# Performance work log

Measured on AMD Instinct MI355X. Metric: run time of the kernel, lower is better.

## Reference

```python
import jax, jax.numpy as jnp
from jax import lax
import numpy as np

B, H, W, C = 8, 56, 56, 384
NUM_HEADS, HEAD_CH = 6, 64
BN_EPS = 1e-5
DN = ('NHWC', 'HWIO', 'NHWC')


def conv_proj(x, dw_kernel, bn_scale, bn_bias, bn_mean, bn_var, pw_kernel, stride):
    """Depthwise conv -> BatchNorm (eval) -> 1x1 pointwise conv, all SAME padding."""
    in_ch = x.shape[-1]
    x = lax.conv_general_dilated(x, dw_kernel, (stride, stride), 'SAME',
                                 dimension_numbers=DN, feature_group_count=in_ch)
    x = (x - bn_mean) * (bn_scale / jnp.sqrt(bn_var + BN_EPS)) + bn_bias
    x = lax.conv_general_dilated(x, pw_kernel, (1, 1), 'SAME', dimension_numbers=DN)
    return x


def setup_inputs() -> dict:
    key = jax.random.key(0)
    ks = jax.random.split(key, 16)
    d = {
        'inputs_q': jax.random.normal(ks[0], (B, H, W, C), jnp.float32),
        'inputs_kv': jax.random.normal(ks[1], (B, H, W, C), jnp.float32),
        'out_kernel': jax.random.normal(ks[2], (NUM_HEADS, HEAD_CH, C), jnp.float32) * 0.05,
    }
    for i, p in enumerate(['q', 'k', 'v']):
        d[f'{p}_dw_kernel'] = jax.random.normal(ks[3 + i], (3, 3, 1, C), jnp.float32) * 0.1
        d[f'{p}_bn_scale'] = jnp.ones((C,), jnp.float32)
        d[f'{p}_bn_bias'] = jnp.zeros((C,), jnp.float32)
        d[f'{p}_bn_mean'] = jnp.zeros((C,), jnp.float32)
        d[f'{p}_bn_var'] = jnp.ones((C,), jnp.float32)
        d[f'{p}_pw_kernel'] = jax.random.normal(ks[6 + i], (1, 1, C, NUM_HEADS * HEAD_CH), jnp.float32) * 0.05
    return d


def reference(inputs_q, inputs_kv,
              q_dw_kernel, q_bn_scale, q_bn_bias, q_bn_mean, q_bn_var, q_pw_kernel,
              k_dw_kernel, k_bn_scale, k_bn_bias, k_bn_mean, k_bn_var, k_pw_kernel,
              v_dw_kernel, v_bn_scale, v_bn_bias, v_bn_mean, v_bn_var, v_pw_kernel,
              out_kernel):
    q = conv_proj(inputs_q, q_dw_kernel, q_bn_scale, q_bn_bias, q_bn_mean, q_bn_var, q_pw_kernel, 1)
    k = conv_proj(inputs_kv, k_dw_kernel, k_bn_scale, k_bn_bias, k_bn_mean, k_bn_var, k_pw_kernel, 2)
    v = conv_proj(inputs_kv, v_dw_kernel, v_bn_scale, v_bn_bias, v_bn_mean, v_bn_var, v_pw_kernel, 2)

    def to_tokens(x):  # [b,H,W,h*d] -> [b,HW,h,d]
        b, hh, ww, _ = x.shape
        return x.reshape(b, hh * ww, NUM_HEADS, HEAD_CH)

    q = to_tokens(q) / jnp.sqrt(jnp.float32(HEAD_CH))
    k = to_tokens(k)
    v = to_tokens(v)

    attn = jnp.einsum('bqhd,bkhd->bhqk', q, k)       # [b,h,Nq,Nkv]
    attn = jax.nn.softmax(attn, axis=-1)
    out = jnp.einsum('bhqk,bkhd->bqhd', attn, v)     # [b,Nq,h,d]
    out = jnp.einsum('bqhd,hdo->bqo', out, out_kernel)  # DenseGeneral over (h,d)
    return out
```

## Files before the change

kernel.cpp:

```cpp
#include <hip/hip_runtime.h>
#include <hip/hip_bf16.h>
#include <hip/hip_fp16.h>

#define BB 8
#define HH 56
#define WW 56
#define CC 384
#define NHD 6
#define DD 64
#define HK 28
#define WK 28
#define NQ (HH*WW)
#define NKV (HK*WK)
#define NTOK (BB*NQ)
#define NTOKKV (BB*NKV)
#define BN_EPS 1e-5f
#define LOG2E 1.44269504f

typedef _Float16 f16;
typedef _Float16 f16x2 __attribute__((ext_vector_type(2)));
typedef _Float16 f16x4 __attribute__((ext_vector_type(4)));
typedef _Float16 f16x8 __attribute__((ext_vector_type(8)));
typedef float f32x4 __attribute__((ext_vector_type(4)));

__device__ __forceinline__ float fast_exp2(float x) {
#if __has_builtin(__builtin_amdgcn_exp2f)
  return __builtin_amdgcn_exp2f(x);
#else
  return __expf(x * 0.69314718056f);
#endif
}

__device__ __forceinline__ f16x4 pack4(float p0, float p1, float p2, float p3) {
#if __has_builtin(__builtin_amdgcn_cvt_pkrtz)
  f16x2 a = __builtin_bit_cast(f16x2, __builtin_amdgcn_cvt_pkrtz(p0, p1));
  f16x2 b = __builtin_bit_cast(f16x2, __builtin_amdgcn_cvt_pkrtz(p2, p3));
  return __builtin_shufflevector(a, b, 0, 1, 2, 3);
#else
  f16x4 r; r[0] = (f16)p0; r[1] = (f16)p1; r[2] = (f16)p2; r[3] = (f16)p3;
  return r;
#endif
}

__device__ __forceinline__ void dw_s1_body(
    int blk, int tid, const float* __restrict__ in, const float* __restrict__ w,
    const float* __restrict__ bns, const float* __restrict__ bnb,
    const float* __restrict__ bnm, const float* __restrict__ bnv,
    f16* __restrict__ out) {
  int idx = blk * 256 + tid;
  int pp = idx / 96;
  int c = (idx % 96) * 4;
  int b = pp / (HH * WK);
  int rem = pp % (HH * WK);
  int y = rem / WK, xh = rem % WK;
  int x0 = xh * 2;
  float a0x = 0, a0y = 0, a0z = 0, a0w = 0;
  float a1x = 0, a1y = 0, a1z = 0, a1w = 0;
#pragma unroll
  for (int kh = 0; kh < 3; ++kh) {
    int iy = y + kh - 1;
    if ((unsigned)iy >= (unsigned)HH) continue;
    const float* rp = in + ((size_t)(b * HH + iy) * WW) * CC + c;
    const float4 z4 = {0.f, 0.f, 0.f, 0.f};
    const float4 v0 = (x0 > 0) ? *(const float4*)(rp + (size_t)(x0 - 1) * CC) : z4;
    const float4 v1 = *(const float4*)(rp + (size_t)x0 * CC);
    const float4 v2 = *(const float4*)(rp + (size_t)(x0 + 1) * CC);
    const float4 v3 = (x0 < 54) ? *(const float4*)(rp + (size_t)(x0 + 2) * CC) : z4;
    const float4 w0 = *(const float4*)(w + (kh * 3 + 0) * CC + c);
    const float4 w1 = *(const float4*)(w + (kh * 3 + 1) * CC + c);
    const float4 w2 = *(const float4*)(w + (kh * 3 + 2) * CC + c);
    a0x = fmaf(v0.x, w0.x, fmaf(v1.x, w1.x, fmaf(v2.x, w2.x, a0x)));
    a0y = fmaf(v0.y, w0.y, fmaf(v1.y, w1.y, fmaf(v2.y, w2.y, a0y)));
    a0z = fmaf(v0.z, w0.z, fmaf(v1.z, w1.z, fmaf(v2.z, w2.z, a0z)));
    a0w = fmaf(v0.w, w0.w, fmaf(v1.w, w1.w, fmaf(v2.w, w2.w, a0w)));
    a1x = fmaf(v1.x, w0.x, fmaf(v2.x, w1.x, fmaf(v3.x, w2.x, a1x)));
    a1y = fmaf(v1.y, w0.y, fmaf(v2.y, w1.y, fmaf(v3.y, w2.y, a1y)));
    a1z = fmaf(v1.z, w0.z, fmaf(v2.z, w1.z, fmaf(v3.z, w2.z, a1z)));
    a1w = fmaf(v1.w, w0.w, fmaf(v2.w, w1.w, fmaf(v3.w, w2.w, a1w)));
  }
  const float4 s = *(const float4*)(bns + c);
  const float4 bi = *(const float4*)(bnb + c);
  const float4 m = *(const float4*)(bnm + c);
  const float4 va = *(const float4*)(bnv + c);
  f16x4 r0, r1;
  float g;
  g = s.x * rsqrtf(va.x + BN_EPS); r0[0] = (f16)fmaf(a0x - m.x, g, bi.x); r1[0] = (f16)fmaf(a1x - m.x, g, bi.x);
  g = s.y * rsqrtf(va.y + BN_EPS); r0[1] = (f16)fmaf(a0y - m.y, g, bi.y); r1[1] = (f16)fmaf(a1y - m.y, g, bi.y);
  g = s.z * rsqrtf(va.z + BN_EPS); r0[2] = (f16)fmaf(a0z - m.z, g, bi.z); r1[2] = (f16)fmaf(a1z - m.z, g, bi.z);
  g = s.w * rsqrtf(va.w + BN_EPS); r0[3] = (f16)fmaf(a0w - m.w, g, bi.w); r1[3] = (f16)fmaf(a1w - m.w, g, bi.w);
  const size_t pix0 = (size_t)b * NQ + y * WW + x0;
  *(f16x4*)(out + pix0 * CC + c) = r0;
  *(f16x4*)(out + (pix0 + 1) * CC + c) = r1;
}

__device__ __forceinline__ void dw_s2_body(
    int blk, int tid, const float* __restrict__ in,
    const float* __restrict__ wk_, const float* __restrict__ kbs, const float* __restrict__ kbb,
    const float* __restrict__ kbm, const float* __restrict__ kbv,
    const float* __restrict__ wv_, const float* __restrict__ vbs, const float* __restrict__ vbb,
    const float* __restrict__ vbm, const float* __restrict__ vbv,
    f16* __restrict__ outk, f16* __restrict__ outv) {
  int idx = blk * 256 + tid;
  int pix = idx / 96;
  int c = (idx % 96) * 4;
  int b = pix / (HK * WK);
  int p = pix % (HK * WK);
  int oy = p / WK, ox = p % WK;
  float kx = 0, ky = 0, kz = 0, kw4 = 0;
  float vx = 0, vy = 0, vz = 0, vw4 = 0;
#pragma unroll
  for (int kh = 0; kh < 3; ++kh) {
    int iy = oy * 2 + kh;
    if (iy >= HH) continue;
#pragma unroll
    for (int kwi = 0; kwi < 3; ++kwi) {
      int ix = ox * 2 + kwi;
      if (ix >= WW) continue;
      const float4 v = *(const float4*)(in + (((size_t)(b * HH + iy) * WW + ix) * CC + c));
      const float4 a = *(const float4*)(wk_ + ((kh * 3 + kwi) * CC + c));
      const float4 bq = *(const float4*)(wv_ + ((kh * 3 + kwi) * CC + c));
      kx = fmaf(v.x, a.x, kx); ky = fmaf(v.y, a.y, ky);
      kz = fmaf(v.z, a.z, kz); kw4 = fmaf(v.w, a.w, kw4);
      vx = fmaf(v.x, bq.x, vx); vy = fmaf(v.y, bq.y, vy);
      vz = fmaf(v.z, bq.z, vz); vw4 = fmaf(v.w, bq.w, vw4);
    }
  }
  {
    const float4 s = *(const float4*)(kbs + c);
    const float4 bi = *(const float4*)(kbb + c);
    const float4 m = *(const float4*)(kbm + c);
    const float4 va = *(const float4*)(kbv + c);
    f16x4 r; float g;
    g = s.x * rsqrtf(va.x + BN_EPS); r[0] = (f16)fmaf(kx - m.x, g, bi.x);
    g = s.y * rsqrtf(va.y + BN_EPS); r[1] = (f16)fmaf(ky - m.y, g, bi.y);
    g = s.z * rsqrtf(va.z + BN_EPS); r[2] = (f16)fmaf(kz - m.z, g, bi.z);
    g = s.w * rsqrtf(va.w + BN_EPS); r[3] = (f16)fmaf(kw4 - m.w, g, bi.w);
    *(f16x4*)(outk + (size_t)pix * CC + c) = r;
  }
  {
    const float4 s = *(const float4*)(vbs + c);
    const float4 bi = *(const float4*)(vbb + c);
    const float4 m = *(const float4*)(vbm + c);
    const float4 va = *(const float4*)(vbv + c);
    f16x4 r; float g;
    g = s.x * rsqrtf(va.x + BN_EPS); r[0] = (f16)fmaf(vx - m.x, g, bi.x);
    g = s.y * rsqrtf(va.y + BN_EPS); r[1] = (f16)fmaf(vy - m.y, g, bi.y);
    g = s.z * rsqrtf(va.z + BN_EPS); r[2] = (f16)fmaf(vz - m.z, g, bi.z);
    g = s.w * rsqrtf(va.w + BN_EPS); r[3] = (f16)fmaf(vw4 - m.w, g, bi.w);
    *(f16x4*)(outv + (size_t)pix * CC + c) = r;
  }
}

__global__ __launch_bounds__(256) void preprocess(
    const float* __restrict__ inputs_q, const float* __restrict__ inputs_kv,
    const float* __restrict__ q_dwk, const float* __restrict__ q_bs,
    const float* __restrict__ q_bb, const float* __restrict__ q_bm,
    const float* __restrict__ q_bv,
    const float* __restrict__ k_dwk, const float* __restrict__ k_bs,
    const float* __restrict__ k_bb, const float* __restrict__ k_bm,
    const float* __restrict__ k_bv,
    const float* __restrict__ v_dwk, const float* __restrict__ v_bs,
    const float* __restrict__ v_bb, const float* __restrict__ v_bm,
    const float* __restrict__ v_bv,
    const float* __restrict__ w0, const float* __restrict__ w1,
    const float* __restrict__ w2, const float* __restrict__ w3,
    f16* __restrict__ o0, f16* __restrict__ o1,
    f16* __restrict__ o2, f16* __restrict__ o3,
    f16* __restrict__ qdw, f16* __restrict__ kdw, f16* __restrict__ vdw) {
  __shared__ float t[32][33];
  const int blk = blockIdx.x;
  const int tid = threadIdx.x;
  if (blk < 4704) {
    dw_s1_body(blk, tid, inputs_q, q_dwk, q_bs, q_bb, q_bm, q_bv, qdw);
  } else if (blk < 7056) {
    dw_s2_body(blk - 4704, tid, inputs_kv,
               k_dwk, k_bs, k_bb, k_bm, k_bv,
               v_dwk, v_bs, v_bb, v_bm, v_bv, kdw, vdw);
  } else {
    const int r = blk - 7056;
    const int z = r / 144, rem = r % 144;
    const int bx = rem % 12, by = rem / 12;
    const float* src = z == 0 ? w0 : z == 1 ? w1 : z == 2 ? w2 : w3;
    f16* dst = z == 0 ? o0 : z == 1 ? o1 : z == 2 ? o2 : o3;
    const int k0 = bx * 32, n0 = by * 32;
    const int x = tid & 31, y = tid >> 5;
#pragma unroll
    for (int i = 0; i < 4; ++i) t[y + i * 8][x] = src[(size_t)(k0 + y + i * 8) * 384 + n0 + x];
    __syncthreads();
#pragma unroll
    for (int i = 0; i < 4; ++i)
      dst[(size_t)(n0 + y + i * 8) * 384 + k0 + x] = (f16)t[x][y + i * 8];
  }
}

template <int MODE>
__device__ __forceinline__ void gemm_body(
    const f16* __restrict__ A, const f16* __restrict__ Bt,
    float* __restrict__ Cf, f16* __restrict__ Ch, float scale,
    int row0, int col0) {
  __shared__ f16 As[128 * 64];
  __shared__ f16 Bs[128 * 64];
  const int tid = threadIdx.x;
  const int wave = tid >> 6, lane = tid & 63;
  const int c = lane & 15, g = lane >> 4;
  const int wr = wave >> 1, wc = wave & 1;

  const int s_base = wave * 64 + lane;
  f32x4 acc[4][4] = {};

  for (int k0 = 0; k0 < 384; k0 += 64) {
    __syncthreads();
#pragma unroll
    for (int j = 0; j < 4; ++j) {
      const int s = j * 256 + s_base;
      const int row = s >> 3, sch = s & 7;
      const int lch = sch ^ (row & 7);
      const f16* sa = A + (size_t)(row0 + row) * 384 + k0 + lch * 8;
      __builtin_amdgcn_global_load_lds(
          (const __attribute__((address_space(1))) void*)sa,
          (__attribute__((address_space(3))) void*)(As + j * 2048 + wave * 512), 16, 0, 0);
      const f16* sb = Bt + (size_t)(col0 + row) * 384 + k0 + lch * 8;
      __builtin_amdgcn_global_load_lds(
          (const __attribute__((address_space(1))) void*)sb,
          (__attribute__((address_space(3))) void*)(Bs + j * 2048 + wave * 512), 16, 0, 0);
    }
    __syncthreads();

#pragma unroll
    for (int kh = 0; kh < 2; ++kh) {
      f16x8 bf[4];
#pragma unroll
      for (int n = 0; n < 4; ++n) {
        const int row = wc * 64 + n * 16 + c;
        bf[n] = *(const f16x8*)(Bs + (size_t)row * 64 + ((kh * 4 + g) ^ (row & 7)) * 8);
      }
#pragma unroll
      for (int m = 0; m < 4; ++m) {
        const int row = wr * 64 + m * 16 + c;
        f16x8 af = *(const f16x8*)(As + (size_t)row * 64 + ((kh * 4 + g) ^ (row & 7)) * 8);
#pragma unroll
        for (int n = 0; n < 4; ++n)
          acc[m][n] = __builtin_amdgcn_mfma_f32_16x16x32_f16(af, bf[n], acc[m][n], 0, 0, 0);
      }
    }
  }

  if (MODE == 2) {
#pragma unroll
    for (int m = 0; m < 4; ++m)
#pragma unroll
      for (int n = 0; n < 4; ++n) {
        const int gr = row0 + wr * 64 + m * 16 + g * 4;
        const int col = col0 + wc * 64 + n * 16 + c;
        const int bb = gr / NKV;
        const int kv = gr - bb * NKV;
        f16x4 pk;
#pragma unroll
        for (int r = 0; r < 4; ++r) pk[r] = (f16)(acc[m][n][r] * scale);
        *(f16x4*)(Ch + ((size_t)bb * 384 + col) * NKV + kv) = pk;
      }
  } else {
#pragma unroll
    for (int m = 0; m < 4; ++m)
#pragma unroll
      for (int n = 0; n < 4; ++n)
#pragma unroll
        for (int r = 0; r < 4; ++r) {
          const size_t row = row0 + wr * 64 + m * 16 + g * 4 + r;
          const size_t col = col0 + wc * 64 + n * 16 + c;
          if (MODE == 1) Ch[row * 384 + col] = (f16)(acc[m][n][r] * scale);
          else           Cf[row * 384 + col] = acc[m][n][r] * scale;
        }
  }
}

__global__ __launch_bounds__(256) void gemm_qkv(
    const f16* __restrict__ qdw, const f16* __restrict__ wqt, f16* __restrict__ qf, float qscale,
    const f16* __restrict__ kdw, const f16* __restrict__ wkt, f16* __restrict__ kf,
    const f16* __restrict__ vdw, const f16* __restrict__ wvt, f16* __restrict__ vtp) {
  const int blk = blockIdx.x;
  if (blk < 588) {
    gemm_body<1>(qdw, wqt, nullptr, qf, qscale, (blk % 196) * 128, (blk / 196) * 128);
  } else if (blk < 735) {
    const int r = blk - 588;
    gemm_body<1>(kdw, wkt, nullptr, kf, 1.0f, (r % 49) * 128, (r / 49) * 128);
  } else {
    const int r = blk - 735;
    gemm_body<2>(vdw, wvt, nullptr, vtp, 1.0f, (r % 49) * 128, (r / 49) * 128);
  }
}

template <int MODE>
__global__ __launch_bounds__(256) void gemm_mfma(
    const f16* __restrict__ A, const f16* __restrict__ Bt,
    float* __restrict__ Cf, f16* __restrict__ Ch, float scale) {
  gemm_body<MODE>(A, Bt, Cf, Ch, scale, blockIdx.x * 128, blockIdx.y * 128);
}

__global__ __launch_bounds__(256) void attn_mfma(
    const f16* __restrict__ qp, const f16* __restrict__ kp,
    const f16* __restrict__ vt, f16* __restrict__ op) {
  __shared__ f16 Ks[64 * 64];
  __shared__ f16 Vs[64 * 64];
  __shared__ f16 Ps[4][16 * 64];
  const int bid0 = blockIdx.x;
  const int lb = (bid0 & 7) * 294 + (bid0 >> 3);
  const int qt = lb % 49;
  const int bh = lb / 49;
  const int h = bh % NHD, b = bh / NHD;
  const int tid = threadIdx.x;
  const int wave = tid >> 6, lane = tid & 63;
  const int c = lane & 15, g = lane >> 4;

  const size_t qrow = (size_t)b * NQ + qt * 64 + wave * 16 + c;
  f16x8 qa[2];
  qa[0] = *(const f16x8*)(qp + qrow * 384 + h * 64 + g * 8);
  qa[1] = *(const f16x8*)(qp + qrow * 384 + h * 64 + 32 + g * 8);

  f16x8 vones;
#pragma unroll
  for (int j = 0; j < 8; ++j) vones[j] = (f16)1.0f;

  const int tid8 = tid >> 3, tch = tid & 7;
  const int lch = tch ^ (tid8 & 7);

  const f16* kbase = kp + ((size_t)b * NKV) * 384 + h * 64;
  const f16* vbase = vt + ((size_t)(b * 384 + h * 64)) * NKV;

  float mrun = -1e30f;
  f32x4 o[4] = {};
  f32x4 osum = {};
  f16* prow = &Ps[wave][0];

  for (int ti = 0; ti < 12; ++ti) {
    const int t0 = ti * 64;
    __syncthreads();
    {
      __builtin_amdgcn_global_load_lds(
          (const __attribute__((address_space(1))) void*)(kbase + (size_t)(t0 + tid8) * 384 + lch * 8),
          (__attribute__((address_space(3))) void*)(Ks + wave * 512), 16, 0, 0);
      __builtin_amdgcn_global_load_lds(
          (const __attribute__((address_space(1))) void*)(kbase + (size_t)(t0 + 32 + tid8) * 384 + lch * 8),
          (__attribute__((address_space(3))) void*)(Ks + 2048 + wave * 512), 16, 0, 0);
      const int col = t0 + lch * 8;
      __builtin_amdgcn_global_load_lds(
          (const __attribute__((address_space(1))) void*)(vbase + (size_t)tid8 * NKV + col),
          (__attribute__((address_space(3))) void*)(Vs + wave * 512), 16, 0, 0);
      __builtin_amdgcn_global_load_lds(
          (const __attribute__((address_space(1))) void*)(vbase + (size_t)(32 + tid8) * NKV + col),
          (__attribute__((address_space(3))) void*)(Vs + 2048 + wave * 512), 16, 0, 0);
    }
    __syncthreads();

    f32x4 s[4] = {};
    __builtin_amdgcn_s_setprio(1);
#pragma unroll
    for (int kh = 0; kh < 2; ++kh) {
#pragma unroll
      for (int ct = 0; ct < 4; ++ct) {
        const int row = ct * 16 + c;
        const int sch = (kh * 4 + g) ^ (row & 7);
        f16x8 kb = *(const f16x8*)(Ks + row * 64 + sch * 8);
        s[ct] = __builtin_amdgcn_mfma_f32_16x16x32_f16(kb, qa[kh], s[ct], 0, 0, 0);
      }
    }
    __builtin_amdgcn_s_setprio(0);

    float mt = s[0][0];
#pragma unroll
    for (int ct = 0; ct < 4; ++ct)
#pragma unroll
      for (int r = 0; r < 4; ++r) mt = fmaxf(mt, s[ct][r]);
    mt = fmaxf(mt, __shfl_xor(mt, 16));
    mt = fmaxf(mt, __shfl_xor(mt, 32));

    if (__ballot(mt > mrun + 8.0f)) {
      const float mnew = fmaxf(mrun, mt);
      const float corr = fast_exp2(mrun - mnew);
      mrun = mnew;
#pragma unroll
      for (int r = 0; r < 4; ++r) {
        const float co = __shfl(corr, g * 4 + r);
#pragma unroll
        for (int dt = 0; dt < 4; ++dt) o[dt][r] *= co;
        osum[r] *= co;
      }
    }

#pragma unroll
    for (int ct = 0; ct < 4; ++ct) {
      const float p0 = fast_exp2(s[ct][0] - mrun);
      const float p1 = fast_exp2(s[ct][1] - mrun);
      const float p2 = fast_exp2(s[ct][2] - mrun);
      const float p3 = fast_exp2(s[ct][3] - mrun);
      const int sch = (ct * 2 + (g >> 1)) ^ (c & 7);
      *(f16x4*)(prow + c * 64 + sch * 8 + (g & 1) * 4) = pack4(p0, p1, p2, p3);
    }

    __builtin_amdgcn_s_setprio(1);
#pragma unroll
    for (int ks = 0; ks < 2; ++ks) {
      const int sp = (ks * 4 + g) ^ (c & 7);
      f16x8 pa = *(const f16x8*)(prow + c * 64 + sp * 8);
#pragma unroll
      for (int dt = 0; dt < 4; ++dt) {
        const int d = dt * 16 + c;
        f16x8 vb = *(const f16x8*)(Vs + d * 64 + sp * 8);
        o[dt] = __builtin_amdgcn_mfma_f32_16x16x32_f16(pa, vb, o[dt], 0, 0, 0);
      }
      osum = __builtin_amdgcn_mfma_f32_16x16x32_f16(pa, vones, osum, 0, 0, 0);
    }
    __builtin_amdgcn_s_setprio(0);
  }

  {
    const int t0 = 768;
    __syncthreads();
    {
      int kv0 = t0 + tid8; if (kv0 > NKV - 1) kv0 = NKV - 1;
      __builtin_amdgcn_global_load_lds(
          (const __attribute__((address_space(1))) void*)(kbase + (size_t)kv0 * 384 + lch * 8),
          (__attribute__((address_space(3))) void*)(Ks + wave * 512), 16, 0, 0);
      int col = t0 + lch * 8; if (col > NKV - 8) col = NKV - 8;
      __builtin_amdgcn_global_load_lds(
          (const __attribute__((address_space(1))) void*)(vbase + (size_t)tid8 * NKV + col),
          (__attribute__((address_space(3))) void*)(Vs + wave * 512), 16, 0, 0);
      __builtin_amdgcn_global_load_lds(
          (const __attribute__((address_space(1))) void*)(vbase + (size_t)(32 + tid8) * NKV + col),
          (__attribute__((address_space(3))) void*)(Vs + 2048 + wave * 512), 16, 0, 0);
    }
    __syncthreads();

    f32x4 s0 = {};
    __builtin_amdgcn_s_setprio(1);
#pragma unroll
    for (int kh = 0; kh < 2; ++kh) {
      const int sch = (kh * 4 + g) ^ (c & 7);
      f16x8 kb = *(const f16x8*)(Ks + c * 64 + sch * 8);
      s0 = __builtin_amdgcn_mfma_f32_16x16x32_f16(kb, qa[kh], s0, 0, 0, 0);
    }
    __builtin_amdgcn_s_setprio(0);

    float mt = fmaxf(fmaxf(s0[0], s0[1]), fmaxf(s0[2], s0[3]));
    mt = fmaxf(mt, __shfl_xor(mt, 16));
    mt = fmaxf(mt, __shfl_xor(mt, 32));
    if (__ballot(mt > mrun + 8.0f)) {
      const float mnew = fmaxf(mrun, mt);
      const float corr = fast_exp2(mrun - mnew);
      mrun = mnew;
#pragma unroll
      for (int r = 0; r < 4; ++r) {
        const float co = __shfl(corr, g * 4 + r);
#pragma unroll
        for (int dt = 0; dt < 4; ++dt) o[dt][r] *= co;
        osum[r] *= co;
      }
    }

    {
      const float p0 = fast_exp2(s0[0] - mrun);
      const float p1 = fast_exp2(s0[1] - mrun);
      const float p2 = fast_exp2(s0[2] - mrun);
      const float p3 = fast_exp2(s0[3] - mrun);
      const int sch0 = (0 + (g >> 1)) ^ (c & 7);
      *(f16x4*)(prow + c * 64 + sch0 * 8 + (g & 1) * 4) = pack4(p0, p1, p2, p3);
      const int sch1 = (2 + (g >> 1)) ^ (c & 7);
      f16x4 z = {};
      *(f16x4*)(prow + c * 64 + sch1 * 8 + (g & 1) * 4) = z;
    }

    __builtin_amdgcn_s_setprio(1);
    {
      const int sp = g ^ (c & 7);
      f16x8 pa = *(const f16x8*)(prow + c * 64 + sp * 8);
#pragma unroll
      for (int dt = 0; dt < 4; ++dt) {
        const int d = dt * 16 + c;
        f16x8 vb = *(const f16x8*)(Vs + d * 64 + sp * 8);
        o[dt] = __builtin_amdgcn_mfma_f32_16x16x32_f16(pa, vb, o[dt], 0, 0, 0);
      }
      osum = __builtin_amdgcn_mfma_f32_16x16x32_f16(pa, vones, osum, 0, 0, 0);
    }
    __builtin_amdgcn_s_setprio(0);
  }

  f16* obase = op + ((size_t)(b * NQ + qt * 64 + wave * 16)) * 384 + h * 64;
#pragma unroll
  for (int r = 0; r < 4; ++r) {
    const float iv = 1.0f / osum[r];
#pragma unroll
    for (int dt = 0; dt < 4; ++dt)
      obase[(size_t)(g * 4 + r) * 384 + dt * 16 + c] = (f16)(o[dt][r] * iv);
  }
}

extern "C" void kernel_launch(void* const* d_in, const int* in_sizes, int n_in,
                              void* d_out, int out_size, void* d_ws, size_t ws_size,
                              hipStream_t stream) {
  const float* inputs_q  = (const float*)d_in[0];
  const float* inputs_kv = (const float*)d_in[1];
  const float* out_kern  = (const float*)d_in[2];
  const float* q_dwk = (const float*)d_in[3];
  const float* q_bs  = (const float*)d_in[4];
  const float* q_bb  = (const float*)d_in[5];
  const float* q_bm  = (const float*)d_in[6];
  const float* q_bv  = (const float*)d_in[7];
  const float* q_pwk = (const float*)d_in[8];
  const float* k_dwk = (const float*)d_in[9];
  const float* k_bs  = (const float*)d_in[10];
  const float* k_bb  = (const float*)d_in[11];
  const float* k_bm  = (const float*)d_in[12];
  const float* k_bv  = (const float*)d_in[13];
  const float* k_pwk = (const float*)d_in[14];
  const float* v_dwk = (const float*)d_in[15];
  const float* v_bs  = (const float*)d_in[16];
  const float* v_bb  = (const float*)d_in[17];
  const float* v_bm  = (const float*)d_in[18];
  const float* v_bv  = (const float*)d_in[19];
  const float* v_pwk = (const float*)d_in[20];

  char* wsb = (char*)d_ws;
  f16* qdw = (f16*)(wsb + 0);
  f16* kdw = (f16*)(wsb + 19267584);
  f16* vdw = (f16*)(wsb + 24084480);
  f16* qf  = (f16*)(wsb + 28901376);
  f16* kf  = (f16*)(wsb + 48168960);
  f16* vtp = (f16*)(wsb + 57802752);
  f16* of  = (f16*)(wsb + 62619648);
  f16* wqt = (f16*)(wsb + 81887232);
  f16* wkt = (f16*)(wsb + 82182144);
  f16* wvt = (f16*)(wsb + 82477056);
  f16* wot = (f16*)(wsb + 82771968);

  preprocess<<<7632, 256, 0, stream>>>(
      inputs_q, inputs_kv,
      q_dwk, q_bs, q_bb, q_bm, q_bv,
      k_dwk, k_bs, k_bb, k_bm, k_bv,
      v_dwk, v_bs, v_bb, v_bm, v_bv,
      q_pwk, k_pwk, v_pwk, out_kern, wqt, wkt, wvt, wot,
      qdw, kdw, vdw);
  gemm_qkv<<<882, 256, 0, stream>>>(qdw, wqt, qf, 0.125f * LOG2E,
                                    kdw, wkt, kf, vdw, wvt, vtp);
  attn_mfma<<<BB * NHD * 49, 256, 0, stream>>>(qf, kf, vtp, of);
  gemm_mfma<0><<<dim3(196, 3), 256, 0, stream>>>(of, wot, (float*)d_out, nullptr, 1.0f);
}
```

Measured before the change: 150.2 us.

## Register-prefetch next K/V tile during attention compute instead of direct LDS loads

Replaces the synchronous global_load_lds staging of each K/V tile with a register-staged software pipeline. The next tile's K and V are loaded into registers while the current tile is computed, then written to LDS at the start of the next iteration. The tail tile is folded into the loop as iteration 13 with clamped indices. The aim is to hide global-load latency behind the MFMA and softmax work, at the cost of extra VGPRs and explicit LDS stores.

```diff
diff --git a/kernel.cpp b/kernel.cpp
--- a/kernel.cpp
+++ b/kernel.cpp
@@ -332,156 +332,143 @@
   f32x4 osum = {};
   f16* prow = &Ps[wave][0];
 
-  for (int ti = 0; ti < 12; ++ti) {
-    const int t0 = ti * 64;
+  f16x8 kr0, kr1, vr0, vr1;
+  kr0 = *(const f16x8*)(kbase + (size_t)tid8 * 384 + lch * 8);
+  kr1 = *(const f16x8*)(kbase + (size_t)(32 + tid8) * 384 + lch * 8);
+  vr0 = *(const f16x8*)(vbase + (size_t)tid8 * NKV + lch * 8);
+  vr1 = *(const f16x8*)(vbase + (size_t)(32 + tid8) * NKV + lch * 8);
+
+  for (int ti = 0; ti < 13; ++ti) {
     __syncthreads();
-    {
-      __builtin_amdgcn_global_load_lds(
-          (const __attribute__((address_space(1))) void*)(kbase + (size_t)(t0 + tid8) * 384 + lch * 8),
-          (__attribute__((address_space(3))) void*)(Ks + wave * 512), 16, 0, 0);
-      __builtin_amdgcn_global_load_lds(
-          (const __attribute__((address_space(1))) void*)(kbase + (size_t)(t0 + 32 + tid8) * 384 + lch * 8),
-          (__attribute__((address_space(3))) void*)(Ks + 2048 + wave * 512), 16, 0, 0);
-      const int col = t0 + lch * 8;
-      __builtin_amdgcn_global_load_lds(
-          (const __attribute__((address_space(1))) void*)(vbase + (size_t)tid8 * NKV + col),
-          (__attribute__((address_space(3))) void*)(Vs + wave * 512), 16, 0, 0);
-      __builtin_amdgcn_global_load_lds(
-          (const __attribute__((address_space(1))) void*)(vbase + (size_t)(32 + tid8) * NKV + col),
-          (__attribute__((address_space(3))) void*)(Vs + 2048 + wave * 512), 16, 0, 0);
+    *(f16x8*)(Ks + tid * 8) = kr0;
+    *(f16x8*)(Ks + 2048 + tid * 8) = kr1;
+    *(f16x8*)(Vs + tid * 8) = vr0;
+    *(f16x8*)(Vs + 2048 + tid * 8) = vr1;
+    if (ti + 1 < 13) {
+      const int t0n = (ti + 1) * 64;
+      int kvA = t0n + tid8;        if (kvA > NKV - 1) kvA = NKV - 1;
+      int kvB = t0n + 32 + tid8;   if (kvB > NKV - 1) kvB = NKV - 1;
+      int colc = t0n + lch * 8;    if (colc > NKV - 8) colc = NKV - 8;
+      kr0 = *(const f16x8*)(kbase + (size_t)kvA * 384 + lch * 8);
+      kr1 = *(const f16x8*)(kbase + (size_t)kvB * 384 + lch * 8);
+      vr0 = *(const f16x8*)(vbase + (size_t)tid8 * NKV + colc);
+      vr1 = *(const f16x8*)(vbase + (size_t)(32 + tid8) * NKV + colc);
     }
     __syncthreads();
 
-    f32x4 s[4] = {};
-    __builtin_amdgcn_s_setprio(1);
-#pragma unroll
-    for (int kh = 0; kh < 2; ++kh) {
+    if (ti < 12) {
+      f32x4 s[4] = {};
+      __builtin_amdgcn_s_setprio(1);
+#pragma unroll
+      for (int kh = 0; kh < 2; ++kh) {
+#pragma unroll
+        for (int ct = 0; ct < 4; ++ct) {
+          const int row = ct * 16 + c;
+          const int sch = (kh * 4 + g) ^ (row & 7);
+          f16x8 kb = *(const f16x8*)(Ks + row * 64 + sch * 8);
+          s[ct] = __builtin_amdgcn_mfma_f32_16x16x32_f16(kb, qa[kh], s[ct], 0, 0, 0);
+        }
+      }
+      __builtin_amdgcn_s_setprio(0);
+
+      float mt = s[0][0];
+#pragma unroll
+      for (int ct = 0; ct < 4; ++ct)
+#pragma unroll
+        for (int r = 0; r < 4; ++r) mt = fmaxf(mt, s[ct][r]);
+      mt = fmaxf(mt, __shfl_xor(mt, 16));
+      mt = fmaxf(mt, __shfl_xor(mt, 32));
+
+      if (__ballot(mt > mrun + 8.0f)) {
+        const float mnew = fmaxf(mrun, mt);
+        const float corr = fast_exp2(mrun - mnew);
+        mrun = mnew;
+#pragma unroll
+        for (int r = 0; r < 4; ++r) {
+          const float co = __shfl(corr, g * 4 + r);
+#pragma unroll
+          for (int dt = 0; dt < 4; ++dt) o[dt][r] *= co;
+          osum[r] *= co;
+        }
+      }
+
 #pragma unroll
       for (int ct = 0; ct < 4; ++ct) {
-        const int row = ct * 16 + c;
-        const int sch = (kh * 4 + g) ^ (row & 7);
-        f16x8 kb = *(const f16x8*)(Ks + row * 64 + sch * 8);
-        s[ct] = __builtin_amdgcn_mfma_f32_16x16x32_f16(kb, qa[kh], s[ct], 0, 0, 0);
-      }
+        const float p0 = fast_exp2(s[ct][0] - mrun);
+        const float p1 = fast_exp2(s[ct][1] - mrun);
+        const float p2 = fast_exp2(s[ct][2] - mrun);
+        const float p3 = fast_exp2(s[ct][3] - mrun);
+        const int sch = (ct * 2 + (g >> 1)) ^ (c & 7);
+        *(f16x4*)(prow + c * 64 + sch * 8 + (g & 1) * 4) = pack4(p0, p1, p2, p3);
+      }
+
+      __builtin_amdgcn_s_setprio(1);
+#pragma unroll
+      for (int ks = 0; ks < 2; ++ks) {
+        const int sp = (ks * 4 + g) ^ (c & 7);
+        f16x8 pa = *(const f16x8*)(prow + c * 64 + sp * 8);
+#pragma unroll
+        for (int dt = 0; dt < 4; ++dt) {
+          const int d = dt * 16 + c;
+          f16x8 vb = *(const f16x8*)(Vs + d * 64 + sp * 8);
+          o[dt] = __builtin_amdgcn_mfma_f32_16x16x32_f16(pa, vb, o[dt], 0, 0, 0);
+        }
+        osum = __builtin_amdgcn_mfma_f32_16x16x32_f16(pa, vones, osum, 0, 0, 0);
+      }
+      __builtin_amdgcn_s_setprio(0);
+    } else {
+      f32x4 s0 = {};
+      __builtin_amdgcn_s_setprio(1);
+#pragma unroll
+      for (int kh = 0; kh < 2; ++kh) {
+        const int sch = (kh * 4 + g) ^ (c & 7);
+        f16x8 kb = *(const f16x8*)(Ks + c * 64 + sch * 8);
+        s0 = __builtin_amdgcn_mfma_f32_16x16x32_f16(kb, qa[kh], s0, 0, 0, 0);
+      }
+      __builtin_amdgcn_s_setprio(0);
+
+      float mt = fmaxf(fmaxf(s0[0], s0[1]), fmaxf(s0[2], s0[3]));
+      mt = fmaxf(mt, __shfl_xor(mt, 16));
+      mt = fmaxf(mt, __shfl_xor(mt, 32));
+      if (__ballot(mt > mrun + 8.0f)) {
+        const float mnew = fmaxf(mrun, mt);
+        const float corr = fast_exp2(mrun - mnew);
+        mrun = mnew;
+#pragma unroll
+        for (int r = 0; r < 4; ++r) {
+          const float co = __shfl(corr, g * 4 + r);
+#pragma unroll
+          for (int dt = 0; dt < 4; ++dt) o[dt][r] *= co;
+          osum[r] *= co;
+        }
+      }
+
+      {
+        const float p0 = fast_exp2(s0[0] - mrun);
+        const float p1 = fast_exp2(s0[1] - mrun);
+        const float p2 = fast_exp2(s0[2] - mrun);
+        const float p3 = fast_exp2(s0[3] - mrun);
+        const int sch0 = (0 + (g >> 1)) ^ (c & 7);
+        *(f16x4*)(prow + c * 64 + sch0 * 8 + (g & 1) * 4) = pack4(p0, p1, p2, p3);
+        const int sch1 = (2 + (g >> 1)) ^ (c & 7);
+        f16x4 z = {};
+        *(f16x4*)(prow + c * 64 + sch1 * 8 + (g & 1) * 4) = z;
+      }
+
+      __builtin_amdgcn_s_setprio(1);
+      {
+        const int sp = g ^ (c & 7);
+        f16x8 pa = *(const f16x8*)(prow + c * 64 + sp * 8);
+#pragma unroll
+        for (int dt = 0; dt < 4; ++dt) {
+          const int d = dt * 16 + c;
+          f16x8 vb = *(const f16x8*)(Vs + d * 64 + sp * 8);
+          o[dt] = __builtin_amdgcn_mfma_f32_16x16x32_f16(pa, vb, o[dt], 0, 0, 0);
+        }
+        osum = __builtin_amdgcn_mfma_f32_16x16x32_f16(pa, vones, osum, 0, 0, 0);
+      }
+      __builtin_amdgcn_s_setprio(0);
     }
-    __builtin_amdgcn_s_setprio(0);
-
-    float mt = s[0][0];
-#pragma unroll
-    for (int ct = 0; ct < 4; ++ct)
-#pragma unroll
-      for (int r = 0; r < 4; ++r) mt = fmaxf(mt, s[ct][r]);
-    mt = fmaxf(mt, __shfl_xor(mt, 16));
-    mt = fmaxf(mt, __shfl_xor(mt, 32));
-
-    if (__ballot(mt > mrun + 8.0f)) {
-      const float mnew = fmaxf(mrun, mt);
-      const float corr = fast_exp2(mrun - mnew);
-      mrun = mnew;
-#pragma unroll
-      for (int r = 0; r < 4; ++r) {
-        const float co = __shfl(corr, g * 4 + r);
-#pragma unroll
-        for (int dt = 0; dt < 4; ++dt) o[dt][r] *= co;
-        osum[r] *= co;
-      }
-    }
-
-#pragma unroll
-    for (int ct = 0; ct < 4; ++ct) {
-      const float p0 = fast_exp2(s[ct][0] - mrun);
-      const float p1 = fast_exp2(s[ct][1] - mrun);
-      const float p2 = fast_exp2(s[ct][2] - mrun);
-      const float p3 = fast_exp2(s[ct][3] - mrun);
-      const int sch = (ct * 2 + (g >> 1)) ^ (c & 7);
-      *(f16x4*)(prow + c * 64 + sch * 8 + (g & 1) * 4) = pack4(p0, p1, p2, p3);
-    }
-
-    __builtin_amdgcn_s_setprio(1);
-#pragma unroll
-    for (int ks = 0; ks < 2; ++ks) {
-      const int sp = (ks * 4 + g) ^ (c & 7);
-      f16x8 pa = *(const f16x8*)(prow + c * 64 + sp * 8);
-#pragma unroll
-      for (int dt = 0; dt < 4; ++dt) {
-        const int d = dt * 16 + c;
-        f16x8 vb = *(const f16x8*)(Vs + d * 64 + sp * 8);
-        o[dt] = __builtin_amdgcn_mfma_f32_16x16x32_f16(pa, vb, o[dt], 0, 0, 0);
-      }
-      osum = __builtin_amdgcn_mfma_f32_16x16x32_f16(pa, vones, osum, 0, 0, 0);
-    }
-    __builtin_amdgcn_s_setprio(0);
-  }
-
-  {
-    const int t0 = 768;
-    __syncthreads();
-    {
-      int kv0 = t0 + tid8; if (kv0 > NKV - 1) kv0 = NKV - 1;
-      __builtin_amdgcn_global_load_lds(
-          (const __attribute__((address_space(1))) void*)(kbase + (size_t)kv0 * 384 + lch * 8),
-          (__attribute__((address_space(3))) void*)(Ks + wave * 512), 16, 0, 0);
-      int col = t0 + lch * 8; if (col > NKV - 8) col = NKV - 8;
-      __builtin_amdgcn_global_load_lds(
-          (const __attribute__((address_space(1))) void*)(vbase + (size_t)tid8 * NKV + col),
-          (__attribute__((address_space(3))) void*)(Vs + wave * 512), 16, 0, 0);
-      __builtin_amdgcn_global_load_lds(
-          (const __attribute__((address_space(1))) void*)(vbase + (size_t)(32 + tid8) * NKV + col),
-          (__attribute__((address_space(3))) void*)(Vs + 2048 + wave * 512), 16, 0, 0);
-    }
-    __syncthreads();
-
-    f32x4 s0 = {};
-    __builtin_amdgcn_s_setprio(1);
-#pragma unroll
-    for (int kh = 0; kh < 2; ++kh) {
-      const int sch = (kh * 4 + g) ^ (c & 7);
-      f16x8 kb = *(const f16x8*)(Ks + c * 64 + sch * 8);
-      s0 = __builtin_amdgcn_mfma_f32_16x16x32_f16(kb, qa[kh], s0, 0, 0, 0);
-    }
-    __builtin_amdgcn_s_setprio(0);
-
-    float mt = fmaxf(fmaxf(s0[0], s0[1]), fmaxf(s0[2], s0[3]));
-    mt = fmaxf(mt, __shfl_xor(mt, 16));
-    mt = fmaxf(mt, __shfl_xor(mt, 32));
-    if (__ballot(mt > mrun + 8.0f)) {
-      const float mnew = fmaxf(mrun, mt);
-      const float corr = fast_exp2(mrun - mnew);
-      mrun = mnew;
-#pragma unroll
-      for (int r = 0; r < 4; ++r) {
-        const float co = __shfl(corr, g * 4 + r);
-#pragma unroll
-        for (int dt = 0; dt < 4; ++dt) o[dt][r] *= co;
-        osum[r] *= co;
-      }
-    }
-
-    {
-      const float p0 = fast_exp2(s0[0] - mrun);
-      const float p1 = fast_exp2(s0[1] - mrun);
-      const float p2 = fast_exp2(s0[2] - mrun);
-      const float p3 = fast_exp2(s0[3] - mrun);
-      const int sch0 = (0 + (g >> 1)) ^ (c & 7);
-      *(f16x4*)(prow + c * 64 + sch0 * 8 + (g & 1) * 4) = pack4(p0, p1, p2, p3);
-      const int sch1 = (2 + (g >> 1)) ^ (c & 7);
-      f16x4 z = {};
-      *(f16x4*)(prow + c * 64 + sch1 * 8 + (g & 1) * 4) = z;
-    }
-
-    __builtin_amdgcn_s_setprio(1);
-    {
-      const int sp = g ^ (c & 7);
-      f16x8 pa = *(const f16x8*)(prow + c * 64 + sp * 8);
-#pragma unroll
-      for (int dt = 0; dt < 4; ++dt) {
-        const int d = dt * 16 + c;
-        f16x8 vb = *(const f16x8*)(Vs + d * 64 + sp * 8);
-        o[dt] = __builtin_amdgcn_mfma_f32_16x16x32_f16(pa, vb, o[dt], 0, 0, 0);
-      }
-      osum = __builtin_amdgcn_mfma_f32_16x16x32_f16(pa, vones, osum, 0, 0, 0);
-    }
-    __builtin_amdgcn_s_setprio(0);
   }
 
   f16* obase = op + ((size_t)(b * NQ + qt * 64 + wave * 16)) * 384 + h * 64;
```

Result: no change. 148.8 us (-0.9%).
